# Performance work log

Hardware: AMD Instinct MI355X
Metric: run time of the kernel (lower is better)

## Reference

```python
import jax, jax.numpy as jnp
import numpy as np
from jax import lax

T = 8192
D_MODEL = 768
D_RNN = 1024
KW = 4  # conv kernel width


def setup_inputs() -> dict:
    key = jax.random.key(0)
    ks = jax.random.split(key, 9)
    x = jax.random.normal(ks[0], (T, D_MODEL), jnp.float32)
    # equinox nn.Linear(in, out): weight [out, in], bias [out]
    w1 = jax.random.normal(ks[1], (2 * D_RNN, D_MODEL), jnp.float32) / np.sqrt(D_MODEL)
    b1 = jnp.zeros((2 * D_RNN,), jnp.float32)
    # nn.Conv1d(d_rnn, d_rnn, 4, use_bias=False): kernel [out_ch, in_ch, kw]
    conv_w = jax.random.normal(ks[2], (D_RNN, D_RNN, KW), jnp.float32) / np.sqrt(D_RNN * KW)
    w_rg = jax.random.normal(ks[3], (2 * D_RNN, D_RNN), jnp.float32) / np.sqrt(D_RNN)
    b_rg = jnp.zeros((2 * D_RNN,), jnp.float32)
    w_out = jax.random.normal(ks[4], (D_MODEL, D_RNN), jnp.float32) / np.sqrt(D_RNN)
    b_out = jnp.zeros((D_MODEL,), jnp.float32)
    # Lambda ~ U(inv_sigmoid(0.9)^{1/8}, inv_sigmoid(0.999)^{1/8}) as in __init__
    inv_sig = lambda p: np.log(1.0 / (1.0 - p))
    lower = np.power(inv_sig(0.9), 1.0 / 8.0)
    upper = np.power(inv_sig(0.999), 1.0 / 8.0)
    Lambda = jax.random.uniform(ks[5], (D_RNN,), jnp.float32, lower, upper)
    return {"x": x, "w1": w1, "b1": b1, "conv_w": conv_w, "w_rg": w_rg,
            "b_rg": b_rg, "w_out": w_out, "b_out": b_out, "Lambda": Lambda}


def _rglru_forward(x, w1, b1, conv_w, w_rg, b_rg, w_out, b_out, Lambda):
    # lin1 then split into gate branch (gelu) and recurrent branch
    h = x @ w1.T + b1                       # [T, 2*D_RNN]
    a_branch = jax.nn.gelu(h[:, :D_RNN])    # [T, D_RNN]
    b_branch = h[:, D_RNN:]                 # [T, D_RNN]
    # causal conv1d: lhs [N=1, C, T], rhs [O, I, KW], left pad 3
    bc = lax.conv_general_dilated(b_branch.T[None], conv_w, (1,), [(KW - 1, 0)])[0].T  # [T, D_RNN]
    # RG-LRU gating
    g = jax.nn.sigmoid(bc @ w_rg.T + b_rg)  # [T, 2*D_RNN]
    inp_gate = g[:, :D_RNN]
    rec_gate = g[:, D_RNN:]
    a_t = jnp.exp(-8.0 * jax.nn.softplus(Lambda)[None, :] * rec_gate)  # [T, D_RNN]
    gated_x = jnp.sqrt(1.0 - a_t ** 2) * inp_gate * bc

    def rec_step(state, xs):
        gx, av = xs
        hn = av * state + gx
        return hn, hn

    _, y = lax.scan(rec_step, jnp.zeros((D_RNN,), x.dtype), (gated_x, a_t))
    return (a_branch * y) @ w_out.T + b_out  # [T, D_MODEL]


def reference(x, w1, b1, conv_w, w_rg, b_rg, w_out, b_out, Lambda):
    return _rglru_forward(x, w1, b1, conv_w, w_rg, b_rg, w_out, b_out, Lambda)
```

## Files before the change

kernel.cpp:

```cpp
#include <hip/hip_runtime.h>
#include <hip/hip_bf16.h>
#include <stdint.h>


#define T_LEN 8192
#define DM 768
#define DR 1024
#define NC 256
#define CL 32

typedef __bf16 bf16x8 __attribute__((ext_vector_type(8)));
typedef float  f32x4  __attribute__((ext_vector_type(4)));

#define AS1 __attribute__((address_space(1)))
#define AS3 __attribute__((address_space(3)))

__device__ __forceinline__ void cp16_g2l(const void* g, void* l) {
    __builtin_amdgcn_global_load_lds((const AS1 void*)g, (AS3 void*)l, 16, 0, 0);
}

__device__ __forceinline__ float gelu_tanh(float x) {
    const float inner = 0.7978845608028654f * (x + 0.044715f * x * x * x);
    return 0.5f * x * (1.f + tanhf(inner));
}

__device__ __forceinline__ __bf16 f2b(float v) {
    __hip_bfloat16 h = __float2bfloat16(v);
    return *reinterpret_cast<__bf16*>(&h);
}

template<int EPI>
__global__ __launch_bounds__(256, 4)
void gemm_mfma(const __hip_bfloat16* __restrict__ A,
               const __hip_bfloat16* __restrict__ WF,
               const float* __restrict__ bias,
               void* __restrict__ Cv,
               int K, int lda, int N,
               __hip_bfloat16* __restrict__ D2)
{
    __shared__ __align__(16) unsigned char smem[32768];
    __bf16* Asb = (__bf16*)smem;

    const int tid  = threadIdx.x;
    const int lane = tid & 63;
    const int wave = tid >> 6;
    const size_t m0 = (size_t)blockIdx.x * 128;
    const int    n0 = blockIdx.y * 64;
    const int wm = (wave >> 1) * 64;
    const int wn = (wave & 1) * 32;

    f32x4 acc[4][2];
#pragma unroll
    for (int i = 0; i < 4; ++i)
#pragma unroll
        for (int j = 0; j < 2; ++j)
            acc[i][j] = f32x4{0.f, 0.f, 0.f, 0.f};

    const int frow = lane & 15;
    const int fq   = lane >> 4;
    const int NKT  = K >> 5;
    const int nt   = K >> 6;

    const __bf16* wbase = (const __bf16*)WF +
        (((size_t)((n0 + wn) >> 4) * NKT) << 9) + (lane << 3);

    auto stageA = [&](int buf, int k0) {
#pragma unroll
        for (int q = 0; q < 4; ++q) {
            const int lin = q * 256 + tid;
            const int rr  = lin >> 3;
            const int gc  = (lin & 7) ^ (rr & 7);
            cp16_g2l(A + (m0 + rr) * (size_t)lda + k0 + gc * 8,
                     Asb + buf * 8192 + lin * 8);
        }
    };

    stageA(0, 0);
#pragma unroll 1
    for (int t = 0; t < nt; ++t) {
        bf16x8 bfr[2][2];
#pragma unroll
        for (int ks = 0; ks < 2; ++ks)
#pragma unroll
            for (int ni = 0; ni < 2; ++ni)
                bfr[ks][ni] = *(const bf16x8*)(wbase +
                    (((size_t)(ni * NKT + 2 * t + ks)) << 9));
        if (t + 1 < nt) {
            stageA((t + 1) & 1, (t + 1) * 64);
            asm volatile("s_waitcnt vmcnt(4)" ::: "memory");
        } else {
            asm volatile("s_waitcnt vmcnt(0)" ::: "memory");
        }
        __builtin_amdgcn_sched_barrier(0);
        __builtin_amdgcn_s_barrier();
        __builtin_amdgcn_sched_barrier(0);

        const int ab = (t & 1) * 8192;
        bf16x8 af[2][4];
#pragma unroll
        for (int ks = 0; ks < 2; ++ks)
#pragma unroll
            for (int mi = 0; mi < 4; ++mi) {
                const int R = wm + mi * 16 + frow;
                af[ks][mi] = *(const bf16x8*)&Asb[ab + R * 64 +
                                                  (((ks * 4 + fq) ^ (R & 7)) * 8)];
            }
        asm volatile("s_waitcnt lgkmcnt(0)" ::: "memory");
        __builtin_amdgcn_sched_barrier(0);
        __builtin_amdgcn_s_setprio(1);
#pragma unroll
        for (int ks = 0; ks < 2; ++ks)
#pragma unroll
            for (int mi = 0; mi < 4; ++mi)
#pragma unroll
                for (int ni = 0; ni < 2; ++ni)
                    acc[mi][ni] = __builtin_amdgcn_mfma_f32_16x16x32_bf16(
                        af[ks][mi], bfr[ks][ni], acc[mi][ni], 0, 0, 0);
        __builtin_amdgcn_s_setprio(0);
        __builtin_amdgcn_sched_barrier(0);
        __builtin_amdgcn_s_barrier();
        __builtin_amdgcn_sched_barrier(0);
    }

    __syncthreads();
    const int er = fq * 4;
    const int ec = frow;

    if (EPI == 0) {
        float* Cl = (float*)smem;
#pragma unroll
        for (int ni = 0; ni < 2; ++ni) {
            const int cc = wn + ni * 16 + ec;
            const float bv = bias ? bias[n0 + cc] : 0.f;
#pragma unroll
            for (int mi = 0; mi < 4; ++mi)
#pragma unroll
                for (int r2 = 0; r2 < 4; ++r2) {
                    const int R = wm + mi * 16 + er + r2;
                    Cl[R * 64 + ((((cc >> 2) ^ (R & 7)) << 2) | (cc & 3))] =
                        acc[mi][ni][r2] + bv;
                }
        }
        __syncthreads();
        float* outp = (float*)Cv;
#pragma unroll
        for (int p = 0; p < 8; ++p) {
            const int R   = (tid >> 4) + p * 16;
            const int chn = tid & 15;
            const f32x4 v = *(const f32x4*)&Cl[R * 64 + ((chn ^ (R & 7)) << 2)];
            *(f32x4*)&outp[(m0 + R) * (size_t)N + n0 + chn * 4] = v;
        }
    } else {
        __bf16* Cl = (__bf16*)smem;
#pragma unroll
        for (int ni = 0; ni < 2; ++ni) {
            const int cc = wn + ni * 16 + ec;
            const float bv = bias ? bias[n0 + cc] : 0.f;
#pragma unroll
            for (int mi = 0; mi < 4; ++mi)
#pragma unroll
                for (int r2 = 0; r2 < 4; ++r2) {
                    const int R = wm + mi * 16 + er + r2;
                    float v = acc[mi][ni][r2] + bv;
                    if (EPI == 2) v = gelu_tanh(v);
                    Cl[R * 64 + ((((cc >> 3) ^ (R & 7)) << 3) | (cc & 7))] = f2b(v);
                }
        }
        __syncthreads();
#pragma unroll
        for (int p = 0; p < 4; ++p) {
            const int R   = (tid >> 3) + p * 32;
            const int chn = tid & 7;
            const bf16x8 v = *(const bf16x8*)&Cl[R * 64 + ((chn ^ (R & 7)) << 3)];
            if (EPI == 1) {
                *(bf16x8*)((__bf16*)Cv + (m0 + R) * (size_t)N + n0 + chn * 8) = v;
            } else if (EPI == 2) {
                *(bf16x8*)((__bf16*)Cv + (m0 + R) * 1024 + n0 + chn * 8) = v;
            } else {
                const int m  = (int)(m0 + R);
                const int s  = m >> 10;
                const int o  = m & 1023;
                const int j  = n0 + chn * 8;
                const size_t dst = (size_t)(o >> 4) * 49152 + (size_t)(j >> 5) * 2048 +
                                   s * 512 + ((((j >> 3) & 3) * 16 + (o & 15)) << 3);
                *(bf16x8*)((__bf16*)Cv + dst) = v;
            }
        }
    }
    (void)D2;
}

__global__ __launch_bounds__(256, 2)
void convx_mfma(const __hip_bfloat16* __restrict__ xbp,
                const __hip_bfloat16* __restrict__ WBf,
                __hip_bfloat16* __restrict__ C)
{
    __shared__ __align__(16) unsigned char smem[32768];
    __bf16* Ah = (__bf16*)smem;

    const int tid  = threadIdx.x;
    const int lane = tid & 63;
    const int wave = tid >> 6;
    const size_t m0 = (size_t)blockIdx.x * 128;
    const int    n0 = blockIdx.y * 128;
    const int wm = (wave >> 1) * 64;
    const int wn = (wave & 1) * 64;

    f32x4 acc[4][4];
#pragma unroll
    for (int i = 0; i < 4; ++i)
#pragma unroll
        for (int j = 0; j < 4; ++j)
            acc[i][j] = f32x4{0.f, 0.f, 0.f, 0.f};

    const int frow = lane & 15;
    const int fq   = lane >> 4;

    const __bf16* wbase = (const __bf16*)WBf +
        (size_t)((n0 + wn) >> 4) * 49152 + (lane << 3);

    auto loadB = [&](bf16x8 (&b)[4][4], int t1) {
#pragma unroll
        for (int s = 0; s < 4; ++s)
#pragma unroll
            for (int ni = 0; ni < 4; ++ni)
                b[s][ni] = *(const bf16x8*)(wbase + (size_t)ni * 49152 +
                                            t1 * 2048 + s * 512);
    };
    auto stageA = [&](int abuf, int kc) {
#pragma unroll
        for (int q = 0; q < 2; ++q) {
            const int lin = q * 256 + tid;
            const int rr  = lin >> 2;
            const int gc  = (lin & 3) ^ ((rr >> 1) & 3);
            cp16_g2l(xbp + (m0 + rr) * 768 + kc + gc * 8, Ah + abuf * 4224 + lin * 8);
        }
        if (tid < 16) {
            const int lin = 512 + tid;
            const int rr  = lin >> 2;
            const int gc  = (lin & 3) ^ ((rr >> 1) & 3);
            cp16_g2l(xbp + (m0 + rr) * 768 + kc + gc * 8, Ah + abuf * 4224 + lin * 8);
        }
    };

    bf16x8 bA[4][4], bB[4][4];
    stageA(0, 0);
    loadB(bA, 0);

    auto iter = [&](bf16x8 (&bCur)[4][4], bf16x8 (&bNxt)[4][4], int t) {
        if (t + 1 < 24) {
            loadB(bNxt, t + 1);
            asm volatile("s_waitcnt vmcnt(16)" ::: "memory");
        } else {
            asm volatile("s_waitcnt vmcnt(0)" ::: "memory");
        }
        __builtin_amdgcn_sched_barrier(0);
        __builtin_amdgcn_s_barrier();
        __builtin_amdgcn_sched_barrier(0);

        const int ab = (t & 1) * 4224;
        __builtin_amdgcn_s_setprio(1);
#pragma unroll
        for (int s = 0; s < 4; ++s) {
            bf16x8 af[4];
#pragma unroll
            for (int mi = 0; mi < 4; ++mi) {
                const int R = wm + mi * 16 + frow + s;
                af[mi] = *(const bf16x8*)&Ah[ab + R * 32 + ((fq ^ ((R >> 1) & 3)) * 8)];
            }
#pragma unroll
            for (int mi = 0; mi < 4; ++mi)
#pragma unroll
                for (int ni = 0; ni < 4; ++ni)
                    acc[mi][ni] = __builtin_amdgcn_mfma_f32_16x16x32_bf16(
                        af[mi], bCur[s][ni], acc[mi][ni], 0, 0, 0);
        }
        __builtin_amdgcn_s_setprio(0);
        __builtin_amdgcn_sched_barrier(0);
        __builtin_amdgcn_s_barrier();
        __builtin_amdgcn_sched_barrier(0);
        if (t + 1 < 24) stageA((t + 1) & 1, (t + 1) * 32);
    };

#pragma unroll 1
    for (int tp = 0; tp < 12; ++tp) {
        iter(bA, bB, 2 * tp);
        iter(bB, bA, 2 * tp + 1);
    }

    __syncthreads();
    const int er = fq * 4;
    const int ec = frow;
    __bf16* Cl = (__bf16*)smem;
#pragma unroll
    for (int ni = 0; ni < 4; ++ni) {
        const int cc = wn + ni * 16 + ec;
#pragma unroll
        for (int mi = 0; mi < 4; ++mi)
#pragma unroll
            for (int r2 = 0; r2 < 4; ++r2) {
                const int R = wm + mi * 16 + er + r2;
                Cl[R * 128 + ((((cc >> 3) ^ (R & 7)) << 3) | (cc & 7))] =
                    f2b(acc[mi][ni][r2]);
            }
    }
    __syncthreads();
#pragma unroll
    for (int p = 0; p < 8; ++p) {
        const int R   = (tid >> 4) + p * 16;
        const int chn = tid & 15;
        const bf16x8 v = *(const bf16x8*)&Cl[R * 128 + ((chn ^ (R & 7)) << 3)];
        *(bf16x8*)((__bf16*)C + (m0 + R) * 1024 + n0 + chn * 8) = v;
    }
}

#define P_XBP  6293760
#define P_W1F  (P_XBP + 786432)
#define P_W1BT (P_W1F + 786432)
#define P_CWR  (P_W1BT + 4194304)
#define P_WRG  (P_CWR + 2097152)
#define P_WO   (P_WRG + 786432)
#define P_TOT  P_WO
__global__ void prep1_kernel(const float* __restrict__ x, const float* __restrict__ w1,
                             const float* __restrict__ w_rg, const float* __restrict__ w_out,
                             const float* __restrict__ conv_w,
                             __hip_bfloat16* __restrict__ xbp, __hip_bfloat16* __restrict__ w1f,
                             __hip_bfloat16* __restrict__ w1bT, __hip_bfloat16* __restrict__ cwr,
                             __hip_bfloat16* __restrict__ w_rgf, __hip_bfloat16* __restrict__ w_outf)
{
    const long e = ((long)blockIdx.x * 256 + threadIdx.x) * 8;
    if (e >= P_TOT) return;
    bf16x8 v;
    if (e < P_XBP) {
        if (e < 2304) {
#pragma unroll
            for (int j = 0; j < 8; ++j) v[j] = f2b(0.f);
        } else {
            const float* s = x + (e - 2304);
#pragma unroll
            for (int j = 0; j < 8; ++j) v[j] = f2b(s[j]);
        }
        *(bf16x8*)&xbp[e] = v;
    } else if (e < P_W1F) {
        const int i  = (int)(e - P_XBP);
        const int nti = i / 12288;
        const int r  = i % 12288;
        const int kt = r >> 9;
        const int l  = (r & 511) >> 3;
        const int row = nti * 16 + (l & 15);
        const int col = kt * 32 + (l >> 4) * 8;
        const float* s = w1 + row * 768 + col;
#pragma unroll
        for (int j = 0; j < 8; ++j) v[j] = f2b(s[j]);
        *(bf16x8*)&w1f[i] = v;
    } else if (e < P_W1BT) {
        const int i  = (int)(e - P_W1F);
        const int nti = i >> 14;
        const int r  = i & 16383;
        const int kt = r >> 9;
        const int l  = (r & 511) >> 3;
        const int jj = nti * 16 + (l & 15);
        const int k0 = kt * 32 + (l >> 4) * 8;
#pragma unroll
        for (int j = 0; j < 8; ++j) v[j] = f2b(w1[(1024 + k0 + j) * 768 + jj]);
        *(bf16x8*)&w1bT[i] = v;
    } else if (e < P_CWR) {
        const int n   = (int)(e - P_W1BT);
        const int row = n >> 10;
        const int i0  = n & 1023;
        const int s   = row >> 10;
        const int o   = row & 1023;
#pragma unroll
        for (int j = 0; j < 8; ++j) v[j] = f2b(conv_w[o * 4096 + (i0 + j) * 4 + s]);
        *(bf16x8*)&cwr[n] = v;
    } else if (e < P_WRG) {
        const int i  = (int)(e - P_CWR);
        const int nti = i >> 14;
        const int r  = i & 16383;
        const int kt = r >> 9;
        const int l  = (r & 511) >> 3;
        const int row = nti * 16 + (l & 15);
        const int col = kt * 32 + (l >> 4) * 8;
        const float* s = w_rg + row * 1024 + col;
#pragma unroll
        for (int j = 0; j < 8; ++j) v[j] = f2b(s[j]);
        *(bf16x8*)&w_rgf[i] = v;
    } else {
        const int i  = (int)(e - P_WRG);
        const int nti = i >> 14;
        const int r  = i & 16383;
        const int kt = r >> 9;
        const int l  = (r & 511) >> 3;
        const int row = nti * 16 + (l & 15);
        const int col = kt * 32 + (l >> 4) * 8;
        const float* s = w_out + row * 1024 + col;
#pragma unroll
        for (int j = 0; j < 8; ++j) v[j] = f2b(s[j]);
        *(bf16x8*)&w_outf[i] = v;
    }
}

__global__ void scan_pass1(const __hip_bfloat16* __restrict__ gp,
                           const __hip_bfloat16* __restrict__ bc,
                           const float* __restrict__ Lambda,
                           float* __restrict__ ch, float* __restrict__ ca)
{
    const int c = blockIdx.y * 256 + threadIdx.x;
    const int j = blockIdx.x;
    const float cl = -8.f * log1pf(expf(Lambda[c]));
    float h = 0.f, ap = 1.f;
    const int t0 = j * CL;
    for (int tt = 0; tt < CL; ++tt) {
        const int t = t0 + tt;
        const long gi = (long)t * 2048 + c;
        const float ig = 1.f / (1.f + expf(-__bfloat162float(gp[gi])));
        const float rg = 1.f / (1.f + expf(-__bfloat162float(gp[gi + 1024])));
        const float a  = expf(cl * rg);
        const float gx = sqrtf(fmaxf(0.f, 1.f - a * a)) * ig *
                         __bfloat162float(bc[(long)t * 1024 + c]);
        h  = fmaf(a, h, gx);
        ap *= a;
    }
    ch[j * 1024 + c] = h;
    ca[j * 1024 + c] = ap;
}

__global__ void scan_combine(float* __restrict__ ch, const float* __restrict__ ca)
{
    const int c = blockIdx.x * 256 + threadIdx.x;
    float carry = 0.f;
    for (int j = 0; j < NC; ++j) {
        const float hj = ch[j * 1024 + c];
        const float aj = ca[j * 1024 + c];
        ch[j * 1024 + c] = carry;
        carry = fmaf(aj, carry, hj);
    }
}

__global__ void scan_pass2(const __hip_bfloat16* __restrict__ gp, const __hip_bfloat16* bc,
                           const float* __restrict__ Lambda,
                           const float* __restrict__ carry_in,
                           const __hip_bfloat16* __restrict__ ab,
                           __hip_bfloat16* zb)
{
    const int c = blockIdx.y * 256 + threadIdx.x;
    const int j = blockIdx.x;
    const float cl = -8.f * log1pf(expf(Lambda[c]));
    float h = carry_in[j * 1024 + c];
    const int t0 = j * CL;
    for (int tt = 0; tt < CL; ++tt) {
        const int t = t0 + tt;
        const long gi = (long)t * 2048 + c;
        const long bi = (long)t * 1024 + c;
        const float ig = 1.f / (1.f + expf(-__bfloat162float(gp[gi])));
        const float rg = 1.f / (1.f + expf(-__bfloat162float(gp[gi + 1024])));
        const float a  = expf(cl * rg);
        const float gx = sqrtf(fmaxf(0.f, 1.f - a * a)) * ig * __bfloat162float(bc[bi]);
        h = fmaf(a, h, gx);
        zb[bi] = __float2bfloat16(__bfloat162float(ab[bi]) * h);
    }
}

extern "C" void kernel_launch(void* const* d_in, const int* in_sizes, int n_in,
                              void* d_out, int out_size, void* d_ws, size_t ws_size,
                              hipStream_t stream)
{
    const float* x      = (const float*)d_in[0];
    const float* w1     = (const float*)d_in[1];
    const float* b1     = (const float*)d_in[2];
    const float* conv_w = (const float*)d_in[3];
    const float* w_rg   = (const float*)d_in[4];
    const float* b_rg   = (const float*)d_in[5];
    const float* w_out  = (const float*)d_in[6];
    const float* b_out  = (const float*)d_in[7];
    const float* Lambda = (const float*)d_in[8];
    float* out = (float*)d_out;
    (void)in_sizes; (void)n_in; (void)out_size; (void)ws_size;

    char* p = (char*)d_ws;
    auto alloc = [&](size_t bytes) { char* r = p; p += (bytes + 255) & ~255ULL; return r; };
    __hip_bfloat16* gpre  = (__hip_bfloat16*)alloc(8192ULL * 2048 * 2);
    __hip_bfloat16* ab    = (__hip_bfloat16*)alloc(8192ULL * 1024 * 2);
    __hip_bfloat16* xbp   = (__hip_bfloat16*)alloc(8200ULL * 768 * 2);
    __hip_bfloat16* bcb   = (__hip_bfloat16*)alloc(8192ULL * 1024 * 2);
    __hip_bfloat16* WBf   = (__hip_bfloat16*)alloc(1024ULL * 4 * 768 * 2);
    __hip_bfloat16* cwr   = (__hip_bfloat16*)alloc(4096ULL * 1024 * 2);
    __hip_bfloat16* w1f   = (__hip_bfloat16*)alloc(1024ULL * 768 * 2);
    __hip_bfloat16* w1bT  = (__hip_bfloat16*)alloc(768ULL * 1024 * 2);
    __hip_bfloat16* w_rgf = (__hip_bfloat16*)alloc(2048ULL * 1024 * 2);
    __hip_bfloat16* w_outf= (__hip_bfloat16*)alloc(768ULL * 1024 * 2);
    float*          chv   = (float*)alloc(NC * 1024ULL * 4);
    float*          cav   = (float*)alloc(NC * 1024ULL * 4);
    __hip_bfloat16* zb    = bcb;

    prep1_kernel<<<(P_TOT / 8 + 255) / 256, 256, 0, stream>>>(
        x, w1, w_rg, w_out, conv_w, xbp, w1f, w1bT, cwr, w_rgf, w_outf);

    {
        dim3 grid(4096 / 128, 768 / 64);
        gemm_mfma<3><<<grid, 256, 0, stream>>>(cwr, w1bT, nullptr, WBf, 1024, 1024, 768, nullptr);
    }

    {
        dim3 grid(T_LEN / 128, 1024 / 64);
        gemm_mfma<2><<<grid, 256, 0, stream>>>(xbp + 2304, w1f, b1, ab, DM, DM, 1024, nullptr);
    }

    {
        dim3 grid(T_LEN / 128, 1024 / 128);
        convx_mfma<<<grid, 256, 0, stream>>>(xbp, WBf, bcb);
    }

    {
        dim3 grid(T_LEN / 128, 2048 / 64);
        gemm_mfma<1><<<grid, 256, 0, stream>>>(bcb, w_rgf, b_rg, gpre, DR, DR, 2048, nullptr);
    }

    {
        dim3 gs(NC, DR / 256);
        scan_pass1<<<gs, 256, 0, stream>>>(gpre, bcb, Lambda, chv, cav);
        scan_combine<<<DR / 256, 256, 0, stream>>>(chv, cav);
        scan_pass2<<<gs, 256, 0, stream>>>(gpre, bcb, Lambda, chv, ab, zb);
    }

    {
        dim3 grid(T_LEN / 128, DM / 64);
        gemm_mfma<0><<<grid, 256, 0, stream>>>(zb, w_outf, b_out, out, DR, DR, DM, nullptr);
    }
}
```

Before: 240.9 us.

## Fuse gelu gate GEMM into conv GEMM and interleave gate columns for scan

```diff
diff --git a/kernel.cpp b/kernel.cpp
--- a/kernel.cpp
+++ b/kernel.cpp
@@ -10,6 +10,7 @@
 #define CL 32
 
 typedef __bf16 bf16x8 __attribute__((ext_vector_type(8)));
+typedef __bf16 bf16x2 __attribute__((ext_vector_type(2)));
 typedef float  f32x4  __attribute__((ext_vector_type(4)));
 
 #define AS1 __attribute__((address_space(1)))
@@ -27,6 +28,10 @@
 __device__ __forceinline__ __bf16 f2b(float v) {
     __hip_bfloat16 h = __float2bfloat16(v);
     return *reinterpret_cast<__bf16*>(&h);
+}
+__device__ __forceinline__ float b2f(__bf16 v) {
+    __hip_bfloat16 h = *reinterpret_cast<__hip_bfloat16*>(&v);
+    return __bfloat162float(h);
 }
 
 template<int EPI>
@@ -161,9 +166,8 @@
 #pragma unroll
                 for (int r2 = 0; r2 < 4; ++r2) {
                     const int R = wm + mi * 16 + er + r2;
-                    float v = acc[mi][ni][r2] + bv;
-                    if (EPI == 2) v = gelu_tanh(v);
-                    Cl[R * 64 + ((((cc >> 3) ^ (R & 7)) << 3) | (cc & 7))] = f2b(v);
+                    Cl[R * 64 + ((((cc >> 3) ^ (R & 7)) << 3) | (cc & 7))] =
+                        f2b(acc[mi][ni][r2] + bv);
                 }
         }
         __syncthreads();
@@ -174,8 +178,6 @@
             const bf16x8 v = *(const bf16x8*)&Cl[R * 64 + ((chn ^ (R & 7)) << 3)];
             if (EPI == 1) {
                 *(bf16x8*)((__bf16*)Cv + (m0 + R) * (size_t)N + n0 + chn * 8) = v;
-            } else if (EPI == 2) {
-                *(bf16x8*)((__bf16*)Cv + (m0 + R) * 1024 + n0 + chn * 8) = v;
             } else {
                 const int m  = (int)(m0 + R);
                 const int s  = m >> 10;
@@ -191,42 +193,41 @@
 }
 
 __global__ __launch_bounds__(256, 2)
-void convx_mfma(const __hip_bfloat16* __restrict__ xbp,
-                const __hip_bfloat16* __restrict__ WBf,
-                __hip_bfloat16* __restrict__ C)
-{
-    __shared__ __align__(16) unsigned char smem[32768];
+void convab_mfma(const __hip_bfloat16* __restrict__ xbp,
+                 const __hip_bfloat16* __restrict__ WBf,
+                 const __hip_bfloat16* __restrict__ W1F,
+                 const float* __restrict__ b1,
+                 __hip_bfloat16* __restrict__ C,
+                 __hip_bfloat16* __restrict__ ABo)
+{
+    __shared__ __align__(16) unsigned char smem[17408];
     __bf16* Ah = (__bf16*)smem;
 
     const int tid  = threadIdx.x;
     const int lane = tid & 63;
     const int wave = tid >> 6;
     const size_t m0 = (size_t)blockIdx.x * 128;
-    const int    n0 = blockIdx.y * 128;
+    const int    n0 = blockIdx.y * 64;
     const int wm = (wave >> 1) * 64;
-    const int wn = (wave & 1) * 64;
-
-    f32x4 acc[4][4];
+    const int wn = (wave & 1) * 32;
+
+    f32x4 acc[4][2], aac[4][2];
 #pragma unroll
     for (int i = 0; i < 4; ++i)
 #pragma unroll
-        for (int j = 0; j < 4; ++j)
+        for (int j = 0; j < 2; ++j) {
             acc[i][j] = f32x4{0.f, 0.f, 0.f, 0.f};
+            aac[i][j] = f32x4{0.f, 0.f, 0.f, 0.f};
+        }
 
     const int frow = lane & 15;
     const int fq   = lane >> 4;
 
-    const __bf16* wbase = (const __bf16*)WBf +
+    const __bf16* wbase  = (const __bf16*)WBf +
         (size_t)((n0 + wn) >> 4) * 49152 + (lane << 3);
-
-    auto loadB = [&](bf16x8 (&b)[4][4], int t1) {
-#pragma unroll
-        for (int s = 0; s < 4; ++s)
-#pragma unroll
-            for (int ni = 0; ni < 4; ++ni)
-                b[s][ni] = *(const bf16x8*)(wbase + (size_t)ni * 49152 +
-                                            t1 * 2048 + s * 512);
-    };
+    const __bf16* w1base = (const __bf16*)W1F +
+        (size_t)((n0 + wn) >> 4) * 12288 + (lane << 3);
+
     auto stageA = [&](int abuf, int kc) {
 #pragma unroll
         for (int q = 0; q < 2; ++q) {
@@ -243,14 +244,22 @@
         }
     };
 
-    bf16x8 bA[4][4], bB[4][4];
     stageA(0, 0);
-    loadB(bA, 0);
-
-    auto iter = [&](bf16x8 (&bCur)[4][4], bf16x8 (&bNxt)[4][4], int t) {
+#pragma unroll 1
+    for (int t = 0; t < 24; ++t) {
+        bf16x8 bfr[4][2], abf[2];
+#pragma unroll
+        for (int s = 0; s < 4; ++s)
+#pragma unroll
+            for (int ni = 0; ni < 2; ++ni)
+                bfr[s][ni] = *(const bf16x8*)(wbase + (size_t)ni * 49152 +
+                                              t * 2048 + s * 512);
+#pragma unroll
+        for (int ni = 0; ni < 2; ++ni)
+            abf[ni] = *(const bf16x8*)(w1base + (size_t)ni * 12288 + t * 512);
         if (t + 1 < 24) {
-            loadB(bNxt, t + 1);
-            asm volatile("s_waitcnt vmcnt(16)" ::: "memory");
+            stageA((t + 1) & 1, (t + 1) * 32);
+            asm volatile("s_waitcnt vmcnt(2)" ::: "memory");
         } else {
             asm volatile("s_waitcnt vmcnt(0)" ::: "memory");
         }
@@ -271,21 +280,22 @@
 #pragma unroll
             for (int mi = 0; mi < 4; ++mi)
 #pragma unroll
-                for (int ni = 0; ni < 4; ++ni)
+                for (int ni = 0; ni < 2; ++ni)
                     acc[mi][ni] = __builtin_amdgcn_mfma_f32_16x16x32_bf16(
-                        af[mi], bCur[s][ni], acc[mi][ni], 0, 0, 0);
+                        af[mi], bfr[s][ni], acc[mi][ni], 0, 0, 0);
+            if (s == 3) {
+#pragma unroll
+                for (int mi = 0; mi < 4; ++mi)
+#pragma unroll
+                    for (int ni = 0; ni < 2; ++ni)
+                        aac[mi][ni] = __builtin_amdgcn_mfma_f32_16x16x32_bf16(
+                            af[mi], abf[ni], aac[mi][ni], 0, 0, 0);
+            }
         }
         __builtin_amdgcn_s_setprio(0);
         __builtin_amdgcn_sched_barrier(0);
         __builtin_amdgcn_s_barrier();
         __builtin_amdgcn_sched_barrier(0);
-        if (t + 1 < 24) stageA((t + 1) & 1, (t + 1) * 32);
-    };
-
-#pragma unroll 1
-    for (int tp = 0; tp < 12; ++tp) {
-        iter(bA, bB, 2 * tp);
-        iter(bB, bA, 2 * tp + 1);
     }
 
     __syncthreads();
@@ -293,24 +303,47 @@
     const int ec = frow;
     __bf16* Cl = (__bf16*)smem;
 #pragma unroll
-    for (int ni = 0; ni < 4; ++ni) {
+    for (int ni = 0; ni < 2; ++ni) {
         const int cc = wn + ni * 16 + ec;
 #pragma unroll
         for (int mi = 0; mi < 4; ++mi)
 #pragma unroll
             for (int r2 = 0; r2 < 4; ++r2) {
                 const int R = wm + mi * 16 + er + r2;
-                Cl[R * 128 + ((((cc >> 3) ^ (R & 7)) << 3) | (cc & 7))] =
+                Cl[R * 64 + ((((cc >> 3) ^ (R & 7)) << 3) | (cc & 7))] =
                     f2b(acc[mi][ni][r2]);
             }
     }
     __syncthreads();
 #pragma unroll
-    for (int p = 0; p < 8; ++p) {
-        const int R   = (tid >> 4) + p * 16;
-        const int chn = tid & 15;
-        const bf16x8 v = *(const bf16x8*)&Cl[R * 128 + ((chn ^ (R & 7)) << 3)];
+    for (int p = 0; p < 4; ++p) {
+        const int R   = (tid >> 3) + p * 32;
+        const int chn = tid & 7;
+        const bf16x8 v = *(const bf16x8*)&Cl[R * 64 + ((chn ^ (R & 7)) << 3)];
         *(bf16x8*)((__bf16*)C + (m0 + R) * 1024 + n0 + chn * 8) = v;
+    }
+
+    __syncthreads();
+#pragma unroll
+    for (int ni = 0; ni < 2; ++ni) {
+        const int cc = wn + ni * 16 + ec;
+        const float bv = b1[n0 + cc];
+#pragma unroll
+        for (int mi = 0; mi < 4; ++mi)
+#pragma unroll
+            for (int r2 = 0; r2 < 4; ++r2) {
+                const int R = wm + mi * 16 + er + r2;
+                Cl[R * 64 + ((((cc >> 3) ^ (R & 7)) << 3) | (cc & 7))] =
+                    f2b(gelu_tanh(aac[mi][ni][r2] + bv));
+            }
+    }
+    __syncthreads();
+#pragma unroll
+    for (int p = 0; p < 4; ++p) {
+        const int R   = (tid >> 3) + p * 32;
+        const int chn = tid & 7;
+        const bf16x8 v = *(const bf16x8*)&Cl[R * 64 + ((chn ^ (R & 7)) << 3)];
+        *(bf16x8*)((__bf16*)ABo + (m0 + R) * 1024 + n0 + chn * 8) = v;
     }
 }
 
@@ -320,13 +353,14 @@
 #define P_CWR  (P_W1BT + 4194304)
 #define P_WRG  (P_CWR + 2097152)
 #define P_WO   (P_WRG + 786432)
-#define P_TOT  P_WO
+#define P_TOT  (P_WO + 2048)
 __global__ void prep1_kernel(const float* __restrict__ x, const float* __restrict__ w1,
                              const float* __restrict__ w_rg, const float* __restrict__ w_out,
-                             const float* __restrict__ conv_w,
+                             const float* __restrict__ conv_w, const float* __restrict__ b_rg,
                              __hip_bfloat16* __restrict__ xbp, __hip_bfloat16* __restrict__ w1f,
                              __hip_bfloat16* __restrict__ w1bT, __hip_bfloat16* __restrict__ cwr,
-                             __hip_bfloat16* __restrict__ w_rgf, __hip_bfloat16* __restrict__ w_outf)
+                             __hip_bfloat16* __restrict__ w_rgf, __hip_bfloat16* __restrict__ w_outf,
+                             float* __restrict__ brgp)
 {
     const long e = ((long)blockIdx.x * 256 + threadIdx.x) * 8;
     if (e >= P_TOT) return;
@@ -380,12 +414,13 @@
         const int kt = r >> 9;
         const int l  = (r & 511) >> 3;
         const int row = nti * 16 + (l & 15);
+        const int src = (row & 1) ? (row >> 1) + 1024 : (row >> 1);
         const int col = kt * 32 + (l >> 4) * 8;
-        const float* s = w_rg + row * 1024 + col;
+        const float* s = w_rg + src * 1024 + col;
 #pragma unroll
         for (int j = 0; j < 8; ++j) v[j] = f2b(s[j]);
         *(bf16x8*)&w_rgf[i] = v;
-    } else {
+    } else if (e < P_WO) {
         const int i  = (int)(e - P_WRG);
         const int nti = i >> 14;
         const int r  = i & 16383;
@@ -397,6 +432,13 @@
 #pragma unroll
         for (int j = 0; j < 8; ++j) v[j] = f2b(s[j]);
         *(bf16x8*)&w_outf[i] = v;
+    } else {
+        const int i0 = (int)(e - P_WO);
+#pragma unroll
+        for (int j = 0; j < 8; ++j) {
+            const int n = i0 + j;
+            brgp[n] = b_rg[(n & 1) ? (n >> 1) + 1024 : (n >> 1)];
+        }
     }
 }
 
@@ -412,9 +454,9 @@
     const int t0 = j * CL;
     for (int tt = 0; tt < CL; ++tt) {
         const int t = t0 + tt;
-        const long gi = (long)t * 2048 + c;
-        const float ig = 1.f / (1.f + expf(-__bfloat162float(gp[gi])));
-        const float rg = 1.f / (1.f + expf(-__bfloat162float(gp[gi + 1024])));
+        const bf16x2 g = *(const bf16x2*)&gp[(long)t * 2048 + 2 * c];
+        const float ig = 1.f / (1.f + expf(-b2f(g[0])));
+        const float rg = 1.f / (1.f + expf(-b2f(g[1])));
         const float a  = expf(cl * rg);
         const float gx = sqrtf(fmaxf(0.f, 1.f - a * a)) * ig *
                          __bfloat162float(bc[(long)t * 1024 + c]);
@@ -450,10 +492,10 @@
     const int t0 = j * CL;
     for (int tt = 0; tt < CL; ++tt) {
         const int t = t0 + tt;
-        const long gi = (long)t * 2048 + c;
         const long bi = (long)t * 1024 + c;
-        const float ig = 1.f / (1.f + expf(-__bfloat162float(gp[gi])));
-        const float rg = 1.f / (1.f + expf(-__bfloat162float(gp[gi + 1024])));
+        const bf16x2 g = *(const bf16x2*)&gp[(long)t * 2048 + 2 * c];
+        const float ig = 1.f / (1.f + expf(-b2f(g[0])));
+        const float rg = 1.f / (1.f + expf(-b2f(g[1])));
         const float a  = expf(cl * rg);
         const float gx = sqrtf(fmaxf(0.f, 1.f - a * a)) * ig * __bfloat162float(bc[bi]);
         h = fmaf(a, h, gx);
@@ -489,12 +531,13 @@
     __hip_bfloat16* w1bT  = (__hip_bfloat16*)alloc(768ULL * 1024 * 2);
     __hip_bfloat16* w_rgf = (__hip_bfloat16*)alloc(2048ULL * 1024 * 2);
     __hip_bfloat16* w_outf= (__hip_bfloat16*)alloc(768ULL * 1024 * 2);
+    float*          brgp  = (float*)alloc(2048ULL * 4);
     float*          chv   = (float*)alloc(NC * 1024ULL * 4);
     float*          cav   = (float*)alloc(NC * 1024ULL * 4);
     __hip_bfloat16* zb    = bcb;
 
     prep1_kernel<<<(P_TOT / 8 + 255) / 256, 256, 0, stream>>>(
-        x, w1, w_rg, w_out, conv_w, xbp, w1f, w1bT, cwr, w_rgf, w_outf);
+        x, w1, w_rg, w_out, conv_w, b_rg, xbp, w1f, w1bT, cwr, w_rgf, w_outf, brgp);
 
     {
         dim3 grid(4096 / 128, 768 / 64);
@@ -503,17 +546,12 @@
 
     {
         dim3 grid(T_LEN / 128, 1024 / 64);
-        gemm_mfma<2><<<grid, 256, 0, stream>>>(xbp + 2304, w1f, b1, ab, DM, DM, 1024, nullptr);
-    }
-
-    {
-        dim3 grid(T_LEN / 128, 1024 / 128);
-        convx_mfma<<<grid, 256, 0, stream>>>(xbp, WBf, bcb);
+        convab_mfma<<<grid, 256, 0, stream>>>(xbp, WBf, w1f, b1, bcb, ab);
     }
 
     {
         dim3 grid(T_LEN / 128, 2048 / 64);
-        gemm_mfma<1><<<grid, 256, 0, stream>>>(bcb, w_rgf, b_rg, gpre, DR, DR, 2048, nullptr);
+        gemm_mfma<1><<<grid, 256, 0, stream>>>(bcb, w_rgf, brgp, gpre, DR, DR, 2048, nullptr);
     }
 
     {
```

After: 246.5 us. 2.3% more time.
